# Kernel optimization log

Hardware: AMD Instinct MI355X
Metric: run time of the kernel (lower is better)

The kernel has to match this reference:

```python
import jax, jax.numpy as jnp
import numpy as np

S, B, I, H = 2048, 64, 256, 512


def setup_inputs() -> dict:
    key = jax.random.key(0)
    ks = jax.random.split(key, 13)
    f = lambda k, sh: jax.random.normal(k, sh, dtype=jnp.float32) * 0.05
    m = lambda k, sh: jax.random.randint(k, sh, 0, 2, dtype=jnp.int32)
    return {
        "x": f(ks[0], (S, B, I)),
        "W_ih0": f(ks[1], (H, I)),
        "W_hh0": f(ks[2], (H, H)),
        "b_ih0": f(ks[3], (H,)),
        "b_hh0": f(ks[4], (H,)),
        "W_ih1": f(ks[5], (H, H)),
        "W_hh1": f(ks[6], (H, H)),
        "b_ih1": f(ks[7], (H,)),
        "b_hh1": f(ks[8], (H,)),
        "mask_ih0": m(ks[9], (H, I)),
        "mask_hh0": m(ks[10], (H, H)),
        "mask_ih1": m(ks[11], (H, H)),
        "mask_hh1": m(ks[12], (H, H)),
    }


def _rnn_layer(x, Wih, Whh, bih, bhh):
    # x: [S, B, in]; tanh RNN layer, h0 = zeros. Precompute input projection
    # for all timesteps (one big GEMM), then scan the recurrence.
    xb = jnp.einsum('sbi,hi->sbh', x, Wih) + bih + bhh  # [S, B, H]

    def step(h, xt):
        h = jnp.tanh(xt + h @ Whh.T)
        return h, h

    h0 = jnp.zeros((x.shape[1], Whh.shape[0]), dtype=x.dtype)
    _, ys = jax.lax.scan(step, h0, xb)
    return ys  # [S, B, H]


def reference(x, W_ih0, W_hh0, b_ih0, b_hh0, W_ih1, W_hh1, b_ih1, b_hh1,
              mask_ih0, mask_hh0, mask_ih1, mask_hh1):
    dt = x.dtype
    y0 = _rnn_layer(x,
                    W_ih0 * mask_ih0.astype(dt), W_hh0 * mask_hh0.astype(dt),
                    b_ih0, b_hh0)
    y1 = _rnn_layer(y0,
                    W_ih1 * mask_ih1.astype(dt), W_hh1 * mask_hh1.astype(dt),
                    b_ih1, b_hh1)
    return y1[-1]  # last timestep hidden state: [B, H]
```

## Files before the change

kernel.cpp:

```cpp
#include <hip/hip_runtime.h>
#include <math.h>

typedef unsigned int u32;
typedef unsigned long long u64;
typedef unsigned short u16;
typedef __attribute__((ext_vector_type(8))) short short8;
typedef __attribute__((ext_vector_type(4))) float f4;
typedef __attribute__((ext_vector_type(4))) u32 u32x4;

#define Ssz 2048
#define Bsz 64
#define Isz 256
#define Hsz 512
#define KC0 24
#define KC1 32

#define WB0_OFF   0u
#define WB1_OFF   1572864u
#define BIAS0_OFF 3670016u
#define BIAS1_OFF 3672064u
#define FLAGS_OFF 3674112u
#define H0_OFF    3675136u
#define H1_OFF    4068352u

#define MFMA(a, b, c) __builtin_amdgcn_mfma_f32_16x16x32_bf16(a, b, c, 0, 0, 0)

__device__ __forceinline__ u16 f2bf(float f) {
  union { float f; u32 u; } v; v.f = f;
  u32 r = v.u + 0x7FFFu + ((v.u >> 16) & 1u);
  return (u16)(r >> 16);
}
__device__ __forceinline__ float bf2f(u16 h) {
  union { u32 u; float f; } v; v.u = ((u32)h) << 16;
  return v.f;
}
__device__ __forceinline__ u32 packbf(float f) {
  u16 hi = f2bf(f);
  u16 lo = f2bf(f - bf2f(hi));
  return (u32)hi | ((u32)lo << 16);
}
__device__ __forceinline__ void unpack2(u32 w0, u32 w1, u32& hi, u32& lo) {
  hi = __builtin_amdgcn_perm(w1, w0, 0x05040100u);
  lo = __builtin_amdgcn_perm(w1, w0, 0x07060302u);
}
__device__ __forceinline__ void cvt2(float a, float b, u32& hi, u32& lo) {
  u16 ha = f2bf(a), hb = f2bf(b);
  u16 la = f2bf(a - bf2f(ha)), lb = f2bf(b - bf2f(hb));
  hi = (u32)ha | ((u32)hb << 16);
  lo = (u32)la | ((u32)lb << 16);
}
__device__ __forceinline__ float ftanh(float xx) {
  float x = fminf(20.f, fmaxf(-20.f, xx));
  float e = __expf(2.f * x);
  return (e - 1.f) / (e + 1.f);
}

union frag { short8 s; u32 w[4]; };

__device__ __forceinline__ u64 ald64(const u64* p) {
  return __hip_atomic_load(p, __ATOMIC_RELAXED, __HIP_MEMORY_SCOPE_AGENT);
}
__device__ __forceinline__ u32 ald32(const u32* p) {
  return __hip_atomic_load(p, __ATOMIC_RELAXED, __HIP_MEMORY_SCOPE_AGENT);
}
__device__ __forceinline__ void ast32(u32* p, u32 v) {
  __hip_atomic_store(p, v, __ATOMIC_RELAXED, __HIP_MEMORY_SCOPE_AGENT);
}

__device__ __forceinline__ void poll1(const u32* f, int tgt) {
  if (tgt <= 0) return;
  while (1) {
    int ok = 1;
    #pragma unroll
    for (int i = 0; i < 8; ++i) ok &= ((int)ald32(f + i) >= tgt);
    if (ok) break;
  }
}
__device__ __forceinline__ void poll2(const u32* f0, int t0, const u32* f1, int t1) {
  if (t0 <= 0 && t1 <= 0) return;
  while (1) {
    int ok = 1;
    #pragma unroll
    for (int i = 0; i < 8; ++i) ok &= ((int)ald32(f0 + i) >= t0);
    #pragma unroll
    for (int i = 0; i < 8; ++i) ok &= ((int)ald32(f1 + i) >= t1);
    if (ok) break;
  }
}

__global__ void prep_weights(const float* __restrict__ Wih0, const float* __restrict__ Whh0,
                             const float* __restrict__ bih0, const float* __restrict__ bhh0,
                             const float* __restrict__ Wih1, const float* __restrict__ Whh1,
                             const float* __restrict__ bih1, const float* __restrict__ bhh1,
                             const int* __restrict__ mih0, const int* __restrict__ mhh0,
                             const int* __restrict__ mih1, const int* __restrict__ mhh1,
                             char* __restrict__ ws) {
  const int L0E = 768 * 512, L1E = 1024 * 512;
  int e = blockIdx.x * blockDim.x + threadIdx.x;
  if (e >= L0E + L1E + 1024) return;
  if (e < L0E) {
    int f = e >> 9, fe = e & 511;
    int lane = fe >> 3, j = fe & 7;
    int n = lane & 15, q = lane >> 4;
    int nt = f / KC0, kc = f % KC0;
    int u = nt * 16 + n, k = kc * 32 + q * 8 + j;
    float w;
    if (k < 256) w = Wih0[u * 256 + k] * (float)mih0[u * 256 + k];
    else         w = Whh0[u * 512 + (k - 256)] * (float)mhh0[u * 512 + (k - 256)];
    ((u32*)(ws + WB0_OFF))[e] = packbf(w);
  } else if (e < L0E + L1E) {
    int e1 = e - L0E;
    int f = e1 >> 9, fe = e1 & 511;
    int lane = fe >> 3, j = fe & 7;
    int n = lane & 15, q = lane >> 4;
    int nt = f >> 5, kc = f & 31;
    int u = nt * 16 + n, k = kc * 32 + q * 8 + j;
    float w;
    if (k < 512) w = Wih1[u * 512 + k] * (float)mih1[u * 512 + k];
    else         w = Whh1[u * 512 + (k - 512)] * (float)mhh1[u * 512 + (k - 512)];
    ((u32*)(ws + WB1_OFF))[e1] = packbf(w);
  } else {
    int b2 = e - L0E - L1E;
    if (b2 < 512) ((float*)(ws + BIAS0_OFF))[b2] = bih0[b2] + bhh0[b2];
    else          ((float*)(ws + BIAS1_OFF))[b2 - 512] = bih1[b2 - 512] + bhh1[b2 - 512];
  }
}


__device__ __forceinline__ void run0(const float* __restrict__ x, char* __restrict__ ws,
                                     int m, int p, int tid, float (*red)[256]) {
  const int w = tid >> 6, lane = tid & 63, n = lane & 15, q = lane >> 4;
  const int nt = p * 4 + (w & 3), ks = w >> 2;
  const int b0 = m * 16;
  const u32* WB = (const u32*)(ws + WB0_OFF);
  u32* flags0 = (u32*)(ws + FLAGS_OFF + m * 256);
  u32* flags1 = flags0 + 16;
  const float bs = ((const float*)(ws + BIAS0_OFF))[nt * 16 + n];

  short8 Whi[12], Wlo[12];
  #pragma unroll
  for (int i = 0; i < 12; ++i) {
    const int kcg = 2 * i + ks;
    const u32* pw = WB + ((nt * KC0 + kcg) * 64 + lane) * 8;
    u32x4 a = *(const u32x4*)pw;
    u32x4 b = *(const u32x4*)(pw + 4);
    frag h, l;
    unpack2(a.x, a.y, h.w[0], l.w[0]);
    unpack2(a.z, a.w, h.w[1], l.w[1]);
    unpack2(b.x, b.y, h.w[2], l.w[2]);
    unpack2(b.z, b.w, h.w[3], l.w[3]);
    Whi[i] = h.s; Wlo[i] = l.s;
  }

  f4 xp[4][2];
  auto loadx = [&](int t) {
    #pragma unroll
    for (int i = 0; i < 4; ++i) {
      const int kcg = 2 * i + ks;
      const float* sx = x + ((long)t * Bsz + b0 + n) * Isz + kcg * 32 + q * 8;
      xp[i][0] = *(const f4*)sx;
      xp[i][1] = *(const f4*)(sx + 4);
    }
  };
  short8 Axh[4], Axl[4];
  auto cvtx = [&]() {
    #pragma unroll
    for (int i = 0; i < 4; ++i) {
      frag h, l;
      #pragma unroll
      for (int v = 0; v < 2; ++v) {
        f4 f = xp[i][v];
        cvt2(f.x, f.y, h.w[2 * v], l.w[2 * v]);
        cvt2(f.z, f.w, h.w[2 * v + 1], l.w[2 * v + 1]);
      }
      Axh[i] = h.s; Axl[i] = l.s;
    }
  };
  loadx(0); cvtx();

  const int cst = (nt * 16 + n) >> 5;
  const int qp = ((nt * 2) + (n >> 3)) & 3;
  const int jj = n & 7;

  for (int t = 0; t < Ssz; ++t) {
    f4 acc = {0.f, 0.f, 0.f, 0.f};
    #pragma unroll
    for (int i = 0; i < 4; ++i) {
      acc = MFMA(Axh[i], Whi[i], acc);
      acc = MFMA(Axh[i], Wlo[i], acc);
      acc = MFMA(Axl[i], Whi[i], acc);
    }
    if (tid == 0) poll2(flags0, t, flags1, t - 2);
    __syncthreads();
    const u32* rb = (const u32*)(ws + H0_OFF) + (((t + 2) % 3) * 4 + m) * 8192;
    u64 hb[8][4];
    #pragma unroll
    for (int i = 0; i < 8; ++i) {
      const u64* pp = (const u64*)(rb + (2 * i + ks) * 512 + lane * 8);
      #pragma unroll
      for (int v = 0; v < 4; ++v) hb[i][v] = ald64(pp + v);
    }
    loadx(t + 1 < Ssz ? t + 1 : t);
    #pragma unroll
    for (int i = 0; i < 8; ++i) {
      frag h, l;
      #pragma unroll
      for (int v = 0; v < 4; ++v)
        unpack2((u32)hb[i][v], (u32)(hb[i][v] >> 32), h.w[v], l.w[v]);
      acc = MFMA(h.s, Whi[4 + i], acc);
      acc = MFMA(h.s, Wlo[4 + i], acc);
      acc = MFMA(l.s, Whi[4 + i], acc);
    }
    *(f4*)&red[w][lane * 4] = acc;
    __syncthreads();
    if (w < 4) {
      u32* wb = (u32*)(ws + H0_OFF) + ((t % 3) * 4 + m) * 8192;
      f4 s0 = *(f4*)&red[w][lane * 4];
      f4 s1 = *(f4*)&red[w + 4][lane * 4];
      #pragma unroll
      for (int r = 0; r < 4; ++r) {
        float val = ftanh(bs + s0[r] + s1[r]);
        ast32(wb + cst * 512 + ((q * 4 + r) + 16 * qp) * 8 + jj, packbf(val));
      }
    }
    __syncthreads();
    if (tid == 0) ast32(flags0 + p, (u32)(t + 1));
    cvtx();
  }
}

__device__ __forceinline__ void run1(char* __restrict__ ws, float* __restrict__ out,
                                     int m, int p, int tid, float (*red)[256]) {
  const int w = tid >> 6, lane = tid & 63, n = lane & 15, q = lane >> 4;
  const int nt = p * 4 + (w & 3), ks = w >> 2;
  const int b0 = m * 16;
  const u32* WB = (const u32*)(ws + WB1_OFF);
  u32* flags0 = (u32*)(ws + FLAGS_OFF + m * 256);
  u32* flags1 = flags0 + 16;
  const float bs = ((const float*)(ws + BIAS1_OFF))[nt * 16 + n];

  short8 Whi[16], Wlo[16];
  #pragma unroll
  for (int i = 0; i < 16; ++i) {
    const int kcg = 2 * i + ks;
    const u32* pw = WB + ((nt * KC1 + kcg) * 64 + lane) * 8;
    u32x4 a = *(const u32x4*)pw;
    u32x4 b = *(const u32x4*)(pw + 4);
    frag h, l;
    unpack2(a.x, a.y, h.w[0], l.w[0]);
    unpack2(a.z, a.w, h.w[1], l.w[1]);
    unpack2(b.x, b.y, h.w[2], l.w[2]);
    unpack2(b.z, b.w, h.w[3], l.w[3]);
    Whi[i] = h.s; Wlo[i] = l.s;
  }

  const int cst = (nt * 16 + n) >> 5;
  const int qp = ((nt * 2) + (n >> 3)) & 3;
  const int jj = n & 7;

  for (int t = 1; t <= Ssz; ++t) {
    if (tid == 0) poll1(flags1, t - 1);
    __syncthreads();
    f4 acc = {0.f, 0.f, 0.f, 0.f};
    {
      const u32* rb = (const u32*)(ws + H1_OFF) + ((t & 1) * 4 + m) * 8192;
      u64 hb[8][4];
      #pragma unroll
      for (int i = 0; i < 8; ++i) {
        const u64* pp = (const u64*)(rb + (2 * i + ks) * 512 + lane * 8);
        #pragma unroll
        for (int v = 0; v < 4; ++v) hb[i][v] = ald64(pp + v);
      }
      #pragma unroll
      for (int i = 0; i < 8; ++i) {
        frag h, l;
        #pragma unroll
        for (int v = 0; v < 4; ++v)
          unpack2((u32)hb[i][v], (u32)(hb[i][v] >> 32), h.w[v], l.w[v]);
        acc = MFMA(h.s, Whi[8 + i], acc);
        acc = MFMA(h.s, Wlo[8 + i], acc);
        acc = MFMA(l.s, Whi[8 + i], acc);
      }
    }
    if (tid == 0) poll1(flags0, t);
    __syncthreads();
    {
      const u32* rb = (const u32*)(ws + H0_OFF) + (((t - 1) % 3) * 4 + m) * 8192;
      u64 hb[8][4];
      #pragma unroll
      for (int i = 0; i < 8; ++i) {
        const u64* pp = (const u64*)(rb + (2 * i + ks) * 512 + lane * 8);
        #pragma unroll
        for (int v = 0; v < 4; ++v) hb[i][v] = ald64(pp + v);
      }
      #pragma unroll
      for (int i = 0; i < 8; ++i) {
        frag h, l;
        #pragma unroll
        for (int v = 0; v < 4; ++v)
          unpack2((u32)hb[i][v], (u32)(hb[i][v] >> 32), h.w[v], l.w[v]);
        acc = MFMA(h.s, Whi[i], acc);
        acc = MFMA(h.s, Wlo[i], acc);
        acc = MFMA(l.s, Whi[i], acc);
      }
    }
    *(f4*)&red[w][lane * 4] = acc;
    __syncthreads();
    if (w < 4) {
      u32* wb = (u32*)(ws + H1_OFF) + (((t - 1) & 1) * 4 + m) * 8192;
      f4 s0 = *(f4*)&red[w][lane * 4];
      f4 s1 = *(f4*)&red[w + 4][lane * 4];
      #pragma unroll
      for (int r = 0; r < 4; ++r) {
        float val = ftanh(bs + s0[r] + s1[r]);
        ast32(wb + cst * 512 + ((q * 4 + r) + 16 * qp) * 8 + jj, packbf(val));
        if (t == Ssz) out[(b0 + q * 4 + r) * Hsz + nt * 16 + n] = val;
      }
    }
    __syncthreads();
    if (tid == 0) ast32(flags1 + p, (u32)t);
  }
}

__global__ __launch_bounds__(512, 2) void rnn_persist(const float* __restrict__ x,
                                                      char* __restrict__ ws,
                                                      float* __restrict__ out) {
  __shared__ float red[8][256];
  const int tid = threadIdx.x;
  const int wg = blockIdx.x;
  const int m = (wg >> 3) & 3, p = wg & 7;
  if (wg < 32) run0(x, ws, m, p, tid, red);
  else         run1(ws, out, m, p, tid, red);
}

extern "C" void kernel_launch(void* const* d_in, const int* in_sizes, int n_in,
                              void* d_out, int out_size, void* d_ws, size_t ws_size,
                              hipStream_t stream) {
  const float* x    = (const float*)d_in[0];
  const float* Wih0 = (const float*)d_in[1];
  const float* Whh0 = (const float*)d_in[2];
  const float* bih0 = (const float*)d_in[3];
  const float* bhh0 = (const float*)d_in[4];
  const float* Wih1 = (const float*)d_in[5];
  const float* Whh1 = (const float*)d_in[6];
  const float* bih1 = (const float*)d_in[7];
  const float* bhh1 = (const float*)d_in[8];
  const int* mih0   = (const int*)d_in[9];
  const int* mhh0   = (const int*)d_in[10];
  const int* mih1   = (const int*)d_in[11];
  const int* mhh1   = (const int*)d_in[12];
  char* ws = (char*)d_ws;

  hipMemsetAsync(ws + FLAGS_OFF, 0, 1024 + 393216 + 262144, stream);

  const int tot = 768 * 512 + 1024 * 512 + 1024;
  prep_weights<<<(tot + 255) / 256, 256, 0, stream>>>(
      Wih0, Whh0, bih0, bhh0, Wih1, Whh1, bih1, bhh1,
      mih0, mhh0, mih1, mhh1, ws);

  rnn_persist<<<64, 512, 0, stream>>>(x, ws, (float*)d_out);
}
```

Measured before the change: 16.18 ms.

## Replace flag polling with parity-tagged hidden-state data for in-band synchronization

Each stored hidden-state word now carries a parity bit, stolen from the low mantissa bit of the bf16 low half, that encodes the timestep. Consumers spin directly on the data loads until every word shows the expected parity, which removes the separate producer flag stores, the consumer flag polls and one __syncthreads per step. Layer 1 also moves its flag publish ahead of the tanh/store, and the MFMA chains are split into two accumulators to expose more ILP. The cost is one bit of precision in the low-order split, plus extra init work that pre-tags the buffers, and correctness now depends on the parity protocol across the triple and double buffers.

```diff
diff --git a/kernel.cpp b/kernel.cpp
--- a/kernel.cpp
+++ b/kernel.cpp
@@ -67,24 +67,23 @@
   __hip_atomic_store(p, v, __ATOMIC_RELAXED, __HIP_MEMORY_SCOPE_AGENT);
 }
 
-__device__ __forceinline__ void poll1(const u32* f, int tgt) {
-  if (tgt <= 0) return;
+__device__ __forceinline__ void spin_load(const u32* rb, int ks, int lane,
+                                          u32 tag, u64 (&hb)[8][4]) {
+  const u64 M = 0x0001000000010000ull;
+  const u64 E = tag ? M : 0ull;
   while (1) {
+    #pragma unroll
+    for (int i = 0; i < 8; ++i) {
+      const u64* pp = (const u64*)(rb + (2 * i + ks) * 512 + lane * 8);
+      #pragma unroll
+      for (int v = 0; v < 4; ++v) hb[i][v] = ald64(pp + v);
+    }
     int ok = 1;
     #pragma unroll
-    for (int i = 0; i < 8; ++i) ok &= ((int)ald32(f + i) >= tgt);
-    if (ok) break;
-  }
-}
-__device__ __forceinline__ void poll2(const u32* f0, int t0, const u32* f1, int t1) {
-  if (t0 <= 0 && t1 <= 0) return;
-  while (1) {
-    int ok = 1;
-    #pragma unroll
-    for (int i = 0; i < 8; ++i) ok &= ((int)ald32(f0 + i) >= t0);
-    #pragma unroll
-    for (int i = 0; i < 8; ++i) ok &= ((int)ald32(f1 + i) >= t1);
-    if (ok) break;
+    for (int i = 0; i < 8; ++i)
+      #pragma unroll
+      for (int v = 0; v < 4; ++v) ok &= (int)((hb[i][v] & M) == E);
+    if (__all(ok)) break;
   }
 }
 
@@ -96,8 +95,9 @@
                              const int* __restrict__ mih1, const int* __restrict__ mhh1,
                              char* __restrict__ ws) {
   const int L0E = 768 * 512, L1E = 1024 * 512;
+  const int TAGN = 3 * 32768;
   int e = blockIdx.x * blockDim.x + threadIdx.x;
-  if (e >= L0E + L1E + 1024) return;
+  if (e >= L0E + L1E + 1024 + TAGN) return;
   if (e < L0E) {
     int f = e >> 9, fe = e & 511;
     int lane = fe >> 3, j = fe & 7;
@@ -119,10 +119,17 @@
     if (k < 512) w = Wih1[u * 512 + k] * (float)mih1[u * 512 + k];
     else         w = Whh1[u * 512 + (k - 512)] * (float)mhh1[u * 512 + (k - 512)];
     ((u32*)(ws + WB1_OFF))[e1] = packbf(w);
-  } else {
+  } else if (e < L0E + L1E + 1024) {
     int b2 = e - L0E - L1E;
     if (b2 < 512) ((float*)(ws + BIAS0_OFF))[b2] = bih0[b2] + bhh0[b2];
     else          ((float*)(ws + BIAS1_OFF))[b2 - 512] = bih1[b2 - 512] + bhh1[b2 - 512];
+  } else {
+    int ti = e - (L0E + L1E + 1024);
+    u32* dst;
+    if (ti < 32768)      dst = (u32*)(ws + H0_OFF) + ti;
+    else if (ti < 65536) dst = (u32*)(ws + H0_OFF) + 32768 + ti;
+    else                 dst = (u32*)(ws + H1_OFF) + (ti - 65536);
+    *dst = 0x00010000u;
   }
 }
 
@@ -133,8 +140,7 @@
   const int nt = p * 4 + (w & 3), ks = w >> 2;
   const int b0 = m * 16;
   const u32* WB = (const u32*)(ws + WB0_OFF);
-  u32* flags0 = (u32*)(ws + FLAGS_OFF + m * 256);
-  u32* flags1 = flags0 + 16;
+  u32* flags1 = (u32*)(ws + FLAGS_OFF + m * 256) + 16;
   const float bs = ((const float*)(ws + BIAS0_OFF))[nt * 16 + n];
 
   short8 Whi[12], Wlo[12];
@@ -181,50 +187,55 @@
   const int cst = (nt * 16 + n) >> 5;
   const int qp = ((nt * 2) + (n >> 3)) & 3;
   const int jj = n & 7;
+  int last1 = 0;
 
   for (int t = 0; t < Ssz; ++t) {
-    f4 acc = {0.f, 0.f, 0.f, 0.f};
+    f4 acc0 = {0.f, 0.f, 0.f, 0.f}, acc1 = {0.f, 0.f, 0.f, 0.f};
     #pragma unroll
     for (int i = 0; i < 4; ++i) {
-      acc = MFMA(Axh[i], Whi[i], acc);
-      acc = MFMA(Axh[i], Wlo[i], acc);
-      acc = MFMA(Axl[i], Whi[i], acc);
-    }
-    if (tid == 0) poll2(flags0, t, flags1, t - 2);
-    __syncthreads();
+      acc0 = MFMA(Axh[i], Whi[i], acc0);
+      acc1 = MFMA(Axh[i], Wlo[i], acc1);
+      acc0 = MFMA(Axl[i], Whi[i], acc0);
+    }
+    loadx(t + 1 < Ssz ? t + 1 : t);
     const u32* rb = (const u32*)(ws + H0_OFF) + (((t + 2) % 3) * 4 + m) * 8192;
     u64 hb[8][4];
-    #pragma unroll
-    for (int i = 0; i < 8; ++i) {
-      const u64* pp = (const u64*)(rb + (2 * i + ks) * 512 + lane * 8);
-      #pragma unroll
-      for (int v = 0; v < 4; ++v) hb[i][v] = ald64(pp + v);
-    }
-    loadx(t + 1 < Ssz ? t + 1 : t);
+    spin_load(rb, ks, lane, (u32)((t + 1) & 1), hb);
     #pragma unroll
     for (int i = 0; i < 8; ++i) {
       frag h, l;
       #pragma unroll
       for (int v = 0; v < 4; ++v)
         unpack2((u32)hb[i][v], (u32)(hb[i][v] >> 32), h.w[v], l.w[v]);
-      acc = MFMA(h.s, Whi[4 + i], acc);
-      acc = MFMA(h.s, Wlo[4 + i], acc);
-      acc = MFMA(l.s, Whi[4 + i], acc);
+      acc0 = MFMA(h.s, Whi[4 + i], acc0);
+      acc1 = MFMA(h.s, Wlo[4 + i], acc1);
+      acc0 = MFMA(l.s, Whi[4 + i], acc0);
+    }
+    f4 acc = acc0 + acc1;
+    if (tid == 0 && last1 < t - 2) {
+      const int tgt = t - 2;
+      while (1) {
+        int mn = 0x7fffffff;
+        #pragma unroll
+        for (int i = 0; i < 8; ++i) { int f = (int)ald32(flags1 + i); if (f < mn) mn = f; }
+        if (mn >= tgt) { last1 = mn; break; }
+      }
     }
     *(f4*)&red[w][lane * 4] = acc;
     __syncthreads();
     if (w < 4) {
       u32* wb = (u32*)(ws + H0_OFF) + ((t % 3) * 4 + m) * 8192;
+      const u32 tb = (u32)(t & 1) << 16;
       f4 s0 = *(f4*)&red[w][lane * 4];
       f4 s1 = *(f4*)&red[w + 4][lane * 4];
       #pragma unroll
       for (int r = 0; r < 4; ++r) {
         float val = ftanh(bs + s0[r] + s1[r]);
-        ast32(wb + cst * 512 + ((q * 4 + r) + 16 * qp) * 8 + jj, packbf(val));
+        u32 pv = (packbf(val) & 0xFFFEFFFFu) | tb;
+        ast32(wb + cst * 512 + ((q * 4 + r) + 16 * qp) * 8 + jj, pv);
       }
     }
     __syncthreads();
-    if (tid == 0) ast32(flags0 + p, (u32)(t + 1));
     cvtx();
   }
 }
@@ -235,8 +246,7 @@
   const int nt = p * 4 + (w & 3), ks = w >> 2;
   const int b0 = m * 16;
   const u32* WB = (const u32*)(ws + WB1_OFF);
-  u32* flags0 = (u32*)(ws + FLAGS_OFF + m * 256);
-  u32* flags1 = flags0 + 16;
+  u32* flags1 = (u32*)(ws + FLAGS_OFF + m * 256) + 16;
   const float bs = ((const float*)(ws + BIAS1_OFF))[nt * 16 + n];
 
   short8 Whi[16], Wlo[16];
@@ -259,66 +269,55 @@
   const int jj = n & 7;
 
   for (int t = 1; t <= Ssz; ++t) {
-    if (tid == 0) poll1(flags1, t - 1);
-    __syncthreads();
-    f4 acc = {0.f, 0.f, 0.f, 0.f};
+    f4 acc0 = {0.f, 0.f, 0.f, 0.f}, acc1 = {0.f, 0.f, 0.f, 0.f};
     {
-      const u32* rb = (const u32*)(ws + H1_OFF) + ((t & 1) * 4 + m) * 8192;
+      const u32* rb = (const u32*)(ws + H0_OFF) + (((t - 1) % 3) * 4 + m) * 8192;
       u64 hb[8][4];
-      #pragma unroll
-      for (int i = 0; i < 8; ++i) {
-        const u64* pp = (const u64*)(rb + (2 * i + ks) * 512 + lane * 8);
-        #pragma unroll
-        for (int v = 0; v < 4; ++v) hb[i][v] = ald64(pp + v);
-      }
+      spin_load(rb, ks, lane, (u32)((t - 1) & 1), hb);
       #pragma unroll
       for (int i = 0; i < 8; ++i) {
         frag h, l;
         #pragma unroll
         for (int v = 0; v < 4; ++v)
           unpack2((u32)hb[i][v], (u32)(hb[i][v] >> 32), h.w[v], l.w[v]);
-        acc = MFMA(h.s, Whi[8 + i], acc);
-        acc = MFMA(h.s, Wlo[8 + i], acc);
-        acc = MFMA(l.s, Whi[8 + i], acc);
-      }
-    }
-    if (tid == 0) poll1(flags0, t);
-    __syncthreads();
+        acc0 = MFMA(h.s, Whi[i], acc0);
+        acc1 = MFMA(h.s, Wlo[i], acc1);
+        acc0 = MFMA(l.s, Whi[i], acc0);
+      }
+    }
     {
-      const u32* rb = (const u32*)(ws + H0_OFF) + (((t - 1) % 3) * 4 + m) * 8192;
+      const u32* rb = (const u32*)(ws + H1_OFF) + ((t & 1) * 4 + m) * 8192;
       u64 hb[8][4];
-      #pragma unroll
-      for (int i = 0; i < 8; ++i) {
-        const u64* pp = (const u64*)(rb + (2 * i + ks) * 512 + lane * 8);
-        #pragma unroll
-        for (int v = 0; v < 4; ++v) hb[i][v] = ald64(pp + v);
-      }
+      spin_load(rb, ks, lane, (u32)(((t - 1) >> 1) & 1), hb);
       #pragma unroll
       for (int i = 0; i < 8; ++i) {
         frag h, l;
         #pragma unroll
         for (int v = 0; v < 4; ++v)
           unpack2((u32)hb[i][v], (u32)(hb[i][v] >> 32), h.w[v], l.w[v]);
-        acc = MFMA(h.s, Whi[i], acc);
-        acc = MFMA(h.s, Wlo[i], acc);
-        acc = MFMA(l.s, Whi[i], acc);
-      }
-    }
+        acc0 = MFMA(h.s, Whi[8 + i], acc0);
+        acc1 = MFMA(h.s, Wlo[8 + i], acc1);
+        acc0 = MFMA(l.s, Whi[8 + i], acc0);
+      }
+    }
+    f4 acc = acc0 + acc1;
     *(f4*)&red[w][lane * 4] = acc;
     __syncthreads();
+    if (tid == 0) ast32(flags1 + p, (u32)t);
     if (w < 4) {
       u32* wb = (u32*)(ws + H1_OFF) + (((t - 1) & 1) * 4 + m) * 8192;
+      const u32 tb = (u32)((t >> 1) & 1) << 16;
       f4 s0 = *(f4*)&red[w][lane * 4];
       f4 s1 = *(f4*)&red[w + 4][lane * 4];
       #pragma unroll
       for (int r = 0; r < 4; ++r) {
         float val = ftanh(bs + s0[r] + s1[r]);
-        ast32(wb + cst * 512 + ((q * 4 + r) + 16 * qp) * 8 + jj, packbf(val));
+        u32 pv = (packbf(val) & 0xFFFEFFFFu) | tb;
+        ast32(wb + cst * 512 + ((q * 4 + r) + 16 * qp) * 8 + jj, pv);
         if (t == Ssz) out[(b0 + q * 4 + r) * Hsz + nt * 16 + n] = val;
       }
     }
     __syncthreads();
-    if (tid == 0) ast32(flags1 + p, (u32)t);
   }
 }
 
@@ -353,7 +352,7 @@
 
   hipMemsetAsync(ws + FLAGS_OFF, 0, 1024 + 393216 + 262144, stream);
 
-  const int tot = 768 * 512 + 1024 * 512 + 1024;
+  const int tot = 768 * 512 + 1024 * 512 + 1024 + 3 * 32768;
   prep_weights<<<(tot + 255) / 256, 256, 0, stream>>>(
       Wih0, Whh0, bih0, bhh0, Wih1, Whh1, bih1, bhh1,
       mih0, mhh0, mih1, mhh1, ws);
```

Measured after the change: 16.10 ms. Within noise of the previous version (-0.5%).
